# Kernel tuning notes

Hardware: AMD Instinct MI355X
Metric: run time of the kernel (lower is better)

The kernel has to match this reference:

```python
import jax, jax.numpy as jnp
import numpy as np

NUM_HEADS = 16
KEY_SIZE = 64
D_MODEL = 1024


def setup_inputs() -> dict:
    key = jax.random.key(0)
    ks = jax.random.split(key, 9)
    B, S = 2, 2048
    HK = NUM_HEADS * KEY_SIZE
    s = 1.0 / np.sqrt(D_MODEL)
    return {
        "x": jax.random.normal(ks[0], (B, S, D_MODEL), dtype=jnp.float32),
        "Wq": jax.random.normal(ks[1], (D_MODEL, HK), dtype=jnp.float32) * s,
        "bq": jax.random.normal(ks[2], (HK,), dtype=jnp.float32) * 0.02,
        "Wk": jax.random.normal(ks[3], (D_MODEL, HK), dtype=jnp.float32) * s,
        "bk": jax.random.normal(ks[4], (HK,), dtype=jnp.float32) * 0.02,
        "Wv": jax.random.normal(ks[5], (D_MODEL, HK), dtype=jnp.float32) * s,
        "bv": jax.random.normal(ks[6], (HK,), dtype=jnp.float32) * 0.02,
        "Wo": jax.random.normal(ks[7], (HK, D_MODEL), dtype=jnp.float32) * s,
        "bo": jax.random.normal(ks[8], (D_MODEL,), dtype=jnp.float32) * 0.02,
    }


def reference(x, Wq, bq, Wk, bk, Wv, bv, Wo, bo):
    B, S, _ = x.shape
    H, K = NUM_HEADS, KEY_SIZE
    # QKV projections -> (B, H, S, K)
    def proj(W, b):
        return (x @ W + b).reshape(B, S, H, K).transpose(0, 2, 1, 3)
    q = proj(Wq, bq)
    k = proj(Wk, bk)
    v = proj(Wv, bv)
    scale = jnp.sqrt(jnp.float32(K))
    scores = jnp.einsum('bhsk,bhtk->bhst', q, k) / scale  # (B,H,S,S)
    attn = jax.nn.softmax(scores, axis=-1)
    out = jnp.einsum('bhst,bhtk->bhsk', attn, v)  # (B,H,S,K)
    out = out.transpose(0, 2, 1, 3).reshape(B, S, H * K)
    return out @ Wo + bo
```

## Files before the change

### kernel.cpp

```cpp
#include <hip/hip_runtime.h>


#define NH 16
#define KS 64
#define DM 1024
#define BB 2
#define SS 2048
#define NT (BB*SS)
#define HKD 1024
#define L2E 1.44269504088896340736f

typedef __attribute__((ext_vector_type(4))) float floatx4;
typedef __attribute__((ext_vector_type(8))) short short8;

#define BAR() asm volatile("s_barrier" ::: "memory")

__device__ __forceinline__ unsigned short f2b(float f) {
  unsigned u = __builtin_bit_cast(unsigned, f);
  u = (u + 0x7fffu + ((u >> 16) & 1u)) >> 16;
  return (unsigned short)u;
}

__device__ __forceinline__ floatx4 mfma16(short8 a, short8 b, floatx4 c) {
  return __builtin_amdgcn_mfma_f32_16x16x32_bf16(a, b, c, 0, 0, 0);
}

__device__ __forceinline__ void async16(const void* g, void* l) {
  __builtin_amdgcn_global_load_lds(
      (const __attribute__((address_space(1))) unsigned int*)g,
      (__attribute__((address_space(3))) unsigned int*)l, 16, 0, 0);
}

__global__ __launch_bounds__(256) void prep_kernel(
    const float* __restrict__ x,
    const float* __restrict__ Wq, const float* __restrict__ Wk,
    const float* __restrict__ Wv, const float* __restrict__ Wo,
    unsigned short* __restrict__ xb,
    unsigned short* __restrict__ wqt, unsigned short* __restrict__ wkt,
    unsigned short* __restrict__ wvt, unsigned short* __restrict__ wot) {
  int bid = blockIdx.x;
  if (bid < NT * DM / 1024) {
    int i = (bid * 256 + threadIdx.x) * 4;
    float4 v = *(const float4*)(x + i);
    ushort4 o;
    o.x = f2b(v.x); o.y = f2b(v.y); o.z = f2b(v.z); o.w = f2b(v.w);
    *(ushort4*)(xb + i) = o;
    return;
  }
  int b2 = bid - NT * DM / 1024;
  int z = b2 >> 8;
  const float* W; unsigned short* Wt;
  if (z == 0)      { W = Wq; Wt = wqt; }
  else if (z == 1) { W = Wk; Wt = wkt; }
  else if (z == 2) { W = Wv; Wt = wvt; }
  else             { W = Wo; Wt = wot; }
  __shared__ __align__(16) unsigned short tile[64][80];
  int k0 = (b2 & 15) * 64, n0 = ((b2 >> 4) & 15) * 64;
  int t = threadIdx.x;
  int c0 = (t & 15) * 4, r = t >> 4;
  #pragma unroll
  for (int p = 0; p < 4; ++p) {
    int rr = r + p * 16;
    float4 v = *(const float4*)(W + (k0 + rr) * DM + n0 + c0);
    tile[c0 + 0][rr] = f2b(v.x);
    tile[c0 + 1][rr] = f2b(v.y);
    tile[c0 + 2][rr] = f2b(v.z);
    tile[c0 + 3][rr] = f2b(v.w);
  }
  __syncthreads();
  int cc0 = (t & 7) * 8, rn = t >> 3;
  #pragma unroll
  for (int p = 0; p < 2; ++p) {
    int nn = rn + p * 32;
    *(short8*)(Wt + (n0 + nn) * DM + k0 + cc0) = *(const short8*)(&tile[nn][cc0]);
  }
}

__global__ __launch_bounds__(256) void gemm_qkv_kernel(
    const unsigned short* __restrict__ xb,
    const unsigned short* __restrict__ wqt, const unsigned short* __restrict__ wkt,
    const unsigned short* __restrict__ wvt,
    const float* __restrict__ bq, const float* __restrict__ bk, const float* __restrict__ bv,
    unsigned short* __restrict__ qb, unsigned short* __restrict__ kbuf,
    unsigned short* __restrict__ vt) {
  __shared__ __align__(16) unsigned short smem[18432];
  const unsigned short* Bt; const float* bias; float scale; int zid = blockIdx.z;
  if (zid == 0)      { Bt = wqt; bias = bq; scale = 0.125f * L2E; }
  else if (zid == 1) { Bt = wkt; bias = bk; scale = 1.0f; }
  else               { Bt = wvt; bias = bv; scale = 1.0f; }
  int m0 = blockIdx.x * 128, n0 = blockIdx.y * 128;
  int t = threadIdx.x, w = t >> 6, lane = t & 63, cl = lane & 15, quad = lane >> 4;
  int wr = (w >> 1) * 64, wc = (w & 1) * 64;
  floatx4 acc[4][4];
  #pragma unroll
  for (int i = 0; i < 4; ++i)
    #pragma unroll
    for (int j = 0; j < 4; ++j)
      acc[i][j] = floatx4{0.f, 0.f, 0.f, 0.f};

  auto stage = [&](int kc, int buf) {
    #pragma unroll
    for (int i = 0; i < 2; ++i) {
      int c = i * 256 + t;
      int row = c >> 2, col = (c & 3) ^ (row & 3);
      async16(xb + (m0 + row) * DM + kc * 32 + col * 8, &smem[buf * 4096 + c * 8]);
      async16(Bt + (n0 + row) * DM + kc * 32 + col * 8, &smem[8192 + buf * 4096 + c * 8]);
    }
  };
  stage(0, 0);
  stage(1, 1);

  for (int kc = 0; kc < DM / 32; ++kc) {
    int cur = kc & 1;
    if (kc < DM / 32 - 1) asm volatile("s_waitcnt vmcnt(4)" ::: "memory");
    else                  asm volatile("s_waitcnt vmcnt(0)" ::: "memory");
    BAR();
    const unsigned short* Ac = &smem[cur * 4096];
    const unsigned short* Bc = &smem[8192 + cur * 4096];
    short8 a[4], b[4];
    #pragma unroll
    for (int i = 0; i < 4; ++i)
      a[i] = *(const short8*)&Ac[(wr + i * 16 + cl) * 32 + ((quad ^ (cl & 3)) * 8)];
    #pragma unroll
    for (int j = 0; j < 4; ++j)
      b[j] = *(const short8*)&Bc[(wc + j * 16 + cl) * 32 + ((quad ^ (cl & 3)) * 8)];
    #pragma unroll
    for (int i = 0; i < 4; ++i)
      #pragma unroll
      for (int j = 0; j < 4; ++j)
        acc[i][j] = mfma16(a[i], b[j], acc[i][j]);
    BAR();
    if (kc + 2 < DM / 32) stage(kc + 2, cur);
  }
  __syncthreads();

  int h = (n0 + wc) >> 6;
  if (zid < 2) {
    unsigned short* dst = (zid == 0) ? qb : kbuf;
    #pragma unroll
    for (int j = 0; j < 4; ++j) {
      float bj = bias[n0 + wc + j * 16 + cl];
      int kd = j * 16 + cl;
      #pragma unroll
      for (int i = 0; i < 4; ++i)
        #pragma unroll
        for (int r = 0; r < 4; ++r) {
          int token = m0 + wr + i * 16 + quad * 4 + r;
          int bz = token >> 11, s = token & (SS - 1);
          float val = (acc[i][j][r] + bj) * scale;
          dst[(((bz * NH + h) * SS + s) << 6) + kd] = f2b(val);
        }
    }
  } else {
    unsigned short* tr = &smem[w * 4608];
    #pragma unroll
    for (int j = 0; j < 4; ++j) {
      float bj = bias[n0 + wc + j * 16 + cl];
      #pragma unroll
      for (int i = 0; i < 4; ++i) {
        unsigned short b0 = f2b(acc[i][j][0] + bj), b1 = f2b(acc[i][j][1] + bj);
        unsigned short b2 = f2b(acc[i][j][2] + bj), b3 = f2b(acc[i][j][3] + bj);
        uint2 pk;
        pk.x = (unsigned)b0 | ((unsigned)b1 << 16);
        pk.y = (unsigned)b2 | ((unsigned)b3 << 16);
        *(uint2*)&tr[(j * 16 + cl) * 72 + i * 16 + quad * 4] = pk;
      }
    }
    asm volatile("s_waitcnt lgkmcnt(0)" ::: "memory");
    int tokbase = m0 + wr;
    int bz = tokbase >> 11, s0 = tokbase & (SS - 1);
    unsigned short* vdst = vt + (((bz * NH + h) * KS) * SS) + s0;
    #pragma unroll
    for (int p = 0; p < 8; ++p) {
      int row = p * 8 + (lane >> 3);
      int tk = (lane & 7) * 8;
      short8 vv = *(const short8*)&tr[row * 72 + tk];
      *(short8*)(vdst + row * SS + tk) = vv;
    }
  }
}

__global__ __launch_bounds__(256) void attn_kernel(
    const unsigned short* __restrict__ Q, const unsigned short* __restrict__ Kb,
    const unsigned short* __restrict__ Vt, unsigned short* __restrict__ AO) {
  __shared__ __align__(16) unsigned short Ks[2][4096], Vs[2][4096];
  __shared__ __align__(16) unsigned short Ps[4][2048];
  int t = threadIdx.x, w = t >> 6, lane = t & 63, cl = lane & 15, quad = lane >> 4;
  int clm = cl & 7;
  int h = blockIdx.y, bz = blockIdx.z, bh = bz * NH + h;
  int q0 = blockIdx.x * 128 + w * 32;
  const unsigned short* Qp = Q + (bh * SS + q0) * KS;
  const unsigned short* Kp = Kb + bh * SS * KS;
  const unsigned short* Vp = Vt + bh * KS * SS;
  unsigned short* p_w = Ps[w];

  short8 qa[2][2];
  #pragma unroll
  for (int qt = 0; qt < 2; ++qt)
    #pragma unroll
    for (int c = 0; c < 2; ++c)
      qa[qt][c] = *(const short8*)(Qp + (qt * 16 + cl) * KS + c * 32 + quad * 8);

  short8 ones;
  #pragma unroll
  for (int j = 0; j < 8; ++j) ones[j] = (short)0x3f80;

  floatx4 lacc[2];
  floatx4 oa[2][4];
  #pragma unroll
  for (int qt = 0; qt < 2; ++qt) {
    lacc[qt] = floatx4{0.f, 0.f, 0.f, 0.f};
    #pragma unroll
    for (int j = 0; j < 4; ++j) oa[qt][j] = floatx4{0.f, 0.f, 0.f, 0.f};
  }

  auto stage = [&](int tile, int buf) {
    #pragma unroll
    for (int i = 0; i < 2; ++i) {
      int c = i * 256 + t;
      int row = c >> 3, col8 = (c & 7) ^ (row & 7);
      async16(Kp + (tile * 64 + row) * KS + col8 * 8, &Ks[buf][c * 8]);
    }
    #pragma unroll
    for (int i = 0; i < 2; ++i) {
      int c = i * 256 + t;
      int d = c >> 3, col8 = (c & 7) ^ (d & 7);
      async16(Vp + d * SS + tile * 64 + col8 * 8, &Vs[buf][c * 8]);
    }
  };
  stage(0, 0);
  stage(1, 1);

  const int NTILES = SS / 64;
  for (int it = 0; it < NTILES; ++it) {
    int cur = it & 1;
    if (it < NTILES - 1) asm volatile("s_waitcnt vmcnt(4)" ::: "memory");
    else                 asm volatile("s_waitcnt vmcnt(0)" ::: "memory");
    BAR();

    floatx4 s[2][4];
    #pragma unroll
    for (int kt = 0; kt < 4; ++kt) {
      short8 kb0 = *(const short8*)&Ks[cur][(kt * 16 + cl) * 64 + ((quad ^ clm) * 8)];
      short8 kb1 = *(const short8*)&Ks[cur][(kt * 16 + cl) * 64 + (((4 + quad) ^ clm) * 8)];
      #pragma unroll
      for (int qt = 0; qt < 2; ++qt) {
        floatx4 z = {0.f, 0.f, 0.f, 0.f};
        s[qt][kt] = mfma16(kb1, qa[qt][1], mfma16(kb0, qa[qt][0], z));
      }
    }
    #pragma unroll
    for (int qt = 0; qt < 2; ++qt)
      #pragma unroll
      for (int kt = 0; kt < 4; ++kt) {
        unsigned u[4];
        #pragma unroll
        for (int r = 0; r < 4; ++r)
          u[r] = __builtin_bit_cast(unsigned, __builtin_amdgcn_exp2f(s[qt][kt][r]));
        uint2 pk;
        pk.x = __builtin_amdgcn_perm(u[1], u[0], 0x07060302);
        pk.y = __builtin_amdgcn_perm(u[3], u[2], 0x07060302);
        int off = qt * 1024 + cl * 64 + (((kt * 2 + (quad >> 1)) ^ clm) * 8) + (quad & 1) * 4;
        *(uint2*)(p_w + off) = pk;
      }
    asm volatile("s_waitcnt lgkmcnt(0)" ::: "memory");
    short8 pa[2][2];
    #pragma unroll
    for (int qt = 0; qt < 2; ++qt) {
      #pragma unroll
      for (int c = 0; c < 2; ++c)
        pa[qt][c] = *(const short8*)(p_w + qt * 1024 + cl * 64 + (((c * 4 + quad) ^ clm) * 8));
      lacc[qt] = mfma16(ones, pa[qt][1], mfma16(ones, pa[qt][0], lacc[qt]));
    }
    #pragma unroll
    for (int j = 0; j < 4; ++j) {
      short8 vb0 = *(const short8*)&Vs[cur][(j * 16 + cl) * 64 + ((quad ^ clm) * 8)];
      short8 vb1 = *(const short8*)&Vs[cur][(j * 16 + cl) * 64 + (((4 + quad) ^ clm) * 8)];
      #pragma unroll
      for (int qt = 0; qt < 2; ++qt)
        oa[qt][j] = mfma16(vb1, pa[qt][1], mfma16(vb0, pa[qt][0], oa[qt][j]));
    }
    BAR();
    if (it + 2 < NTILES) stage(it + 2, cur);
  }

  #pragma unroll
  for (int qt = 0; qt < 2; ++qt) {
    float inv = 1.0f / lacc[qt][0];
    unsigned short* aop = AO + (bz * SS + q0 + qt * 16 + cl) * DM + h * KS + quad * 4;
    #pragma unroll
    for (int j = 0; j < 4; ++j) {
      unsigned short b0 = f2b(oa[qt][j][0] * inv), b1 = f2b(oa[qt][j][1] * inv);
      unsigned short b2 = f2b(oa[qt][j][2] * inv), b3 = f2b(oa[qt][j][3] * inv);
      uint2 pk;
      pk.x = (unsigned)b0 | ((unsigned)b1 << 16);
      pk.y = (unsigned)b2 | ((unsigned)b3 << 16);
      *(uint2*)(aop + j * 16) = pk;
    }
  }
}

__global__ __launch_bounds__(256) void gemm_out_kernel(
    const unsigned short* __restrict__ ao, const unsigned short* __restrict__ wot,
    const float* __restrict__ bo, float* __restrict__ out) {
  __shared__ __align__(16) unsigned short As[2][8192], Bs[2][2048];
  int m0 = blockIdx.x * 256, n0 = blockIdx.y * 64;
  int t = threadIdx.x, w = t >> 6, lane = t & 63, cl = lane & 15, quad = lane >> 4;
  int wr = w * 64;
  floatx4 acc[4][4];
  #pragma unroll
  for (int i = 0; i < 4; ++i)
    #pragma unroll
    for (int j = 0; j < 4; ++j)
      acc[i][j] = floatx4{0.f, 0.f, 0.f, 0.f};

  auto stage = [&](int kc, int buf) {
    #pragma unroll
    for (int i = 0; i < 4; ++i) {
      int c = i * 256 + t;
      int row = c >> 2, col = (c & 3) ^ (row & 3);
      async16(ao + (m0 + row) * HKD + kc * 32 + col * 8, &As[buf][c * 8]);
    }
    {
      int c = t;
      int row = c >> 2, col = (c & 3) ^ (row & 3);
      async16(wot + (n0 + row) * HKD + kc * 32 + col * 8, &Bs[buf][c * 8]);
    }
  };
  stage(0, 0);
  stage(1, 1);

  for (int kc = 0; kc < HKD / 32; ++kc) {
    int cur = kc & 1;
    if (kc < HKD / 32 - 1) asm volatile("s_waitcnt vmcnt(5)" ::: "memory");
    else                   asm volatile("s_waitcnt vmcnt(0)" ::: "memory");
    BAR();
    short8 a[4], b[4];
    #pragma unroll
    for (int i = 0; i < 4; ++i)
      a[i] = *(const short8*)&As[cur][(wr + i * 16 + cl) * 32 + ((quad ^ (cl & 3)) * 8)];
    #pragma unroll
    for (int j = 0; j < 4; ++j)
      b[j] = *(const short8*)&Bs[cur][(j * 16 + cl) * 32 + ((quad ^ (cl & 3)) * 8)];
    #pragma unroll
    for (int i = 0; i < 4; ++i)
      #pragma unroll
      for (int j = 0; j < 4; ++j)
        acc[i][j] = mfma16(a[i], b[j], acc[i][j]);
    BAR();
    if (kc + 2 < HKD / 32) stage(kc + 2, cur);
  }
  #pragma unroll
  for (int j = 0; j < 4; ++j) {
    float bj = bo[n0 + j * 16 + cl];
    #pragma unroll
    for (int i = 0; i < 4; ++i)
      #pragma unroll
      for (int r = 0; r < 4; ++r) {
        int token = m0 + wr + i * 16 + quad * 4 + r;
        out[token * DM + n0 + j * 16 + cl] = acc[i][j][r] + bj;
      }
  }
}

extern "C" void kernel_launch(void* const* d_in, const int* in_sizes, int n_in,
                              void* d_out, int out_size, void* d_ws, size_t ws_size,
                              hipStream_t stream) {
  const float* x  = (const float*)d_in[0];
  const float* Wq = (const float*)d_in[1];
  const float* bq = (const float*)d_in[2];
  const float* Wk = (const float*)d_in[3];
  const float* bk = (const float*)d_in[4];
  const float* Wv = (const float*)d_in[5];
  const float* bv = (const float*)d_in[6];
  const float* Wo = (const float*)d_in[7];
  const float* bo = (const float*)d_in[8];
  float* out = (float*)d_out;
  char* ws = (char*)d_ws;
  unsigned short* xb  = (unsigned short*)(ws);
  unsigned short* wqt = (unsigned short*)(ws + (8ull  << 20));
  unsigned short* wkt = (unsigned short*)(ws + (10ull << 20));
  unsigned short* wvt = (unsigned short*)(ws + (12ull << 20));
  unsigned short* wot = (unsigned short*)(ws + (14ull << 20));
  unsigned short* qb  = (unsigned short*)(ws + (16ull << 20));
  unsigned short* kbf = (unsigned short*)(ws + (24ull << 20));
  unsigned short* vt  = (unsigned short*)(ws + (40ull << 20));
  unsigned short* ao  = (unsigned short*)(ws + (48ull << 20));

  hipLaunchKernelGGL(prep_kernel, dim3(NT * DM / 1024 + 1024), dim3(256), 0, stream,
                     x, Wq, Wk, Wv, Wo, xb, wqt, wkt, wvt, wot);
  hipLaunchKernelGGL(gemm_qkv_kernel, dim3(NT / 128, HKD / 128, 3), dim3(256), 0, stream,
                     xb, wqt, wkt, wvt, bq, bk, bv, qb, kbf, vt);
  hipLaunchKernelGGL(attn_kernel, dim3(SS / 128, NH, BB), dim3(256), 0, stream, qb, kbf, vt, ao);
  hipLaunchKernelGGL(gemm_out_kernel, dim3(NT / 256, DM / 64), dim3(256), 0, stream, ao, wot, bo, out);
}
```

Measured before the change: 202.2 us.

## Split attention key range across two wave groups with LDS reduction

The attention kernel now runs 512 threads per block. Two groups of four waves each process half of the key sequence for the same 128 queries, using 32-key tiles. At the end the partial outputs and row sums are combined through shared memory before normalization. The aim is more waves in flight to hide latency, since the grid of 512 blocks is small relative to the CU count. The cost is an extra LDS reduction and barrier, smaller tiles per iteration, and possibly lower occupancy per CU.

Measured after the change: 197.7 us. 2.2% less time.

```diff
diff --git a/kernel.cpp b/kernel.cpp
--- a/kernel.cpp
+++ b/kernel.cpp
@@ -180,19 +180,19 @@
   }
 }
 
-__global__ __launch_bounds__(256) void attn_kernel(
+__global__ __launch_bounds__(512) void attn_kernel(
     const unsigned short* __restrict__ Q, const unsigned short* __restrict__ Kb,
     const unsigned short* __restrict__ Vt, unsigned short* __restrict__ AO) {
-  __shared__ __align__(16) unsigned short Ks[2][4096], Vs[2][4096];
-  __shared__ __align__(16) unsigned short Ps[4][2048];
+  __shared__ __align__(16) unsigned short smem[24576];
   int t = threadIdx.x, w = t >> 6, lane = t & 63, cl = lane & 15, quad = lane >> 4;
-  int clm = cl & 7;
+  int clm = cl & 7, cl3 = cl & 3, cl2 = cl >> 2;
   int h = blockIdx.y, bz = blockIdx.z, bh = bz * NH + h;
-  int q0 = blockIdx.x * 128 + w * 32;
+  int slice = w & 3, part = w >> 2;
+  int q0 = blockIdx.x * 128 + slice * 32;
   const unsigned short* Qp = Q + (bh * SS + q0) * KS;
   const unsigned short* Kp = Kb + bh * SS * KS;
   const unsigned short* Vp = Vt + bh * KS * SS;
-  unsigned short* p_w = Ps[w];
+  unsigned short* p_w = smem + 16384 + w * 1024;
 
   short8 qa[2][2];
   #pragma unroll
@@ -214,35 +214,32 @@
     for (int j = 0; j < 4; ++j) oa[qt][j] = floatx4{0.f, 0.f, 0.f, 0.f};
   }
 
-  auto stage = [&](int tile, int buf) {
-    #pragma unroll
-    for (int i = 0; i < 2; ++i) {
-      int c = i * 256 + t;
-      int row = c >> 3, col8 = (c & 7) ^ (row & 7);
-      async16(Kp + (tile * 64 + row) * KS + col8 * 8, &Ks[buf][c * 8]);
-    }
-    #pragma unroll
-    for (int i = 0; i < 2; ++i) {
-      int c = i * 256 + t;
-      int d = c >> 3, col8 = (c & 7) ^ (d & 7);
-      async16(Vp + d * SS + tile * 64 + col8 * 8, &Vs[buf][c * 8]);
-    }
+  int st = t >> 8, lt = t & 255;
+  int krow = lt >> 3, kcol = (lt & 7) ^ (krow & 7);
+  int vd = lt >> 2, vcol = ((lt & 3) ^ (vd & 3) ^ ((vd >> 2) & 3)) & 3;
+  auto stage = [&](int it, int buf) {
+    async16(Kp + (st * 1024 + it * 32 + krow) * KS + kcol * 8,
+            &smem[(st * 2 + buf) * 2048 + lt * 8]);
+    async16(Vp + vd * SS + st * 1024 + it * 32 + vcol * 8,
+            &smem[8192 + (st * 2 + buf) * 2048 + lt * 8]);
   };
   stage(0, 0);
   stage(1, 1);
 
-  const int NTILES = SS / 64;
-  for (int it = 0; it < NTILES; ++it) {
+  const int NIT = 1024 / 32;
+  for (int it = 0; it < NIT; ++it) {
     int cur = it & 1;
-    if (it < NTILES - 1) asm volatile("s_waitcnt vmcnt(4)" ::: "memory");
-    else                 asm volatile("s_waitcnt vmcnt(0)" ::: "memory");
-    BAR();
-
-    floatx4 s[2][4];
-    #pragma unroll
-    for (int kt = 0; kt < 4; ++kt) {
-      short8 kb0 = *(const short8*)&Ks[cur][(kt * 16 + cl) * 64 + ((quad ^ clm) * 8)];
-      short8 kb1 = *(const short8*)&Ks[cur][(kt * 16 + cl) * 64 + (((4 + quad) ^ clm) * 8)];
+    if (it < NIT - 1) asm volatile("s_waitcnt vmcnt(2)" ::: "memory");
+    else              asm volatile("s_waitcnt vmcnt(0)" ::: "memory");
+    BAR();
+    const unsigned short* Kc = &smem[(part * 2 + cur) * 2048];
+    const unsigned short* Vc = &smem[8192 + (part * 2 + cur) * 2048];
+
+    floatx4 s[2][2];
+    #pragma unroll
+    for (int kt = 0; kt < 2; ++kt) {
+      short8 kb0 = *(const short8*)&Kc[(kt * 16 + cl) * 64 + ((quad ^ clm) * 8)];
+      short8 kb1 = *(const short8*)&Kc[(kt * 16 + cl) * 64 + (((4 + quad) ^ clm) * 8)];
       #pragma unroll
       for (int qt = 0; qt < 2; ++qt) {
         floatx4 z = {0.f, 0.f, 0.f, 0.f};
@@ -252,7 +249,7 @@
     #pragma unroll
     for (int qt = 0; qt < 2; ++qt)
       #pragma unroll
-      for (int kt = 0; kt < 4; ++kt) {
+      for (int kt = 0; kt < 2; ++kt) {
         unsigned u[4];
         #pragma unroll
         for (int r = 0; r < 4; ++r)
@@ -260,42 +257,63 @@
         uint2 pk;
         pk.x = __builtin_amdgcn_perm(u[1], u[0], 0x07060302);
         pk.y = __builtin_amdgcn_perm(u[3], u[2], 0x07060302);
-        int off = qt * 1024 + cl * 64 + (((kt * 2 + (quad >> 1)) ^ clm) * 8) + (quad & 1) * 4;
+        int blk = ((kt * 2 + (quad >> 1)) ^ cl3 ^ cl2) & 3;
+        int off = qt * 512 + cl * 32 + blk * 8 + (quad & 1) * 4;
         *(uint2*)(p_w + off) = pk;
       }
     asm volatile("s_waitcnt lgkmcnt(0)" ::: "memory");
-    short8 pa[2][2];
+    short8 pa[2];
     #pragma unroll
     for (int qt = 0; qt < 2; ++qt) {
-      #pragma unroll
-      for (int c = 0; c < 2; ++c)
-        pa[qt][c] = *(const short8*)(p_w + qt * 1024 + cl * 64 + (((c * 4 + quad) ^ clm) * 8));
-      lacc[qt] = mfma16(ones, pa[qt][1], mfma16(ones, pa[qt][0], lacc[qt]));
+      pa[qt] = *(const short8*)(p_w + qt * 512 + cl * 32 + (((quad ^ cl3 ^ cl2) & 3) * 8));
+      lacc[qt] = mfma16(ones, pa[qt], lacc[qt]);
     }
     #pragma unroll
     for (int j = 0; j < 4; ++j) {
-      short8 vb0 = *(const short8*)&Vs[cur][(j * 16 + cl) * 64 + ((quad ^ clm) * 8)];
-      short8 vb1 = *(const short8*)&Vs[cur][(j * 16 + cl) * 64 + (((4 + quad) ^ clm) * 8)];
+      short8 vb = *(const short8*)&Vc[(j * 16 + cl) * 32 + (((quad ^ cl3 ^ cl2) & 3) * 8)];
       #pragma unroll
       for (int qt = 0; qt < 2; ++qt)
-        oa[qt][j] = mfma16(vb1, pa[qt][1], mfma16(vb0, pa[qt][0], oa[qt][j]));
-    }
-    BAR();
-    if (it + 2 < NTILES) stage(it + 2, cur);
-  }
-
-  #pragma unroll
-  for (int qt = 0; qt < 2; ++qt) {
-    float inv = 1.0f / lacc[qt][0];
-    unsigned short* aop = AO + (bz * SS + q0 + qt * 16 + cl) * DM + h * KS + quad * 4;
-    #pragma unroll
-    for (int j = 0; j < 4; ++j) {
-      unsigned short b0 = f2b(oa[qt][j][0] * inv), b1 = f2b(oa[qt][j][1] * inv);
-      unsigned short b2 = f2b(oa[qt][j][2] * inv), b3 = f2b(oa[qt][j][3] * inv);
-      uint2 pk;
-      pk.x = (unsigned)b0 | ((unsigned)b1 << 16);
-      pk.y = (unsigned)b2 | ((unsigned)b3 << 16);
-      *(uint2*)(aop + j * 16) = pk;
+        oa[qt][j] = mfma16(vb, pa[qt], oa[qt][j]);
+    }
+    BAR();
+    if (it + 2 < NIT) stage(it + 2, cur);
+  }
+
+  __syncthreads();
+  float* red = (float*)smem;
+  float* base = red + slice * 2304;
+  if (part == 1) {
+    #pragma unroll
+    for (int qt = 0; qt < 2; ++qt)
+      #pragma unroll
+      for (int j = 0; j < 4; ++j)
+        *(floatx4*)(base + (((qt * 4 + j) * 64 + lane) << 2)) = oa[qt][j];
+    base[2048 + lane * 2 + 0] = lacc[0][0];
+    base[2048 + lane * 2 + 1] = lacc[1][0];
+  }
+  __syncthreads();
+  if (part == 0) {
+    #pragma unroll
+    for (int qt = 0; qt < 2; ++qt)
+      #pragma unroll
+      for (int j = 0; j < 4; ++j)
+        oa[qt][j] += *(const floatx4*)(base + (((qt * 4 + j) * 64 + lane) << 2));
+    float lsum[2];
+    lsum[0] = lacc[0][0] + base[2048 + lane * 2 + 0];
+    lsum[1] = lacc[1][0] + base[2048 + lane * 2 + 1];
+    #pragma unroll
+    for (int qt = 0; qt < 2; ++qt) {
+      float inv = 1.0f / lsum[qt];
+      unsigned short* aop = AO + (bz * SS + q0 + qt * 16 + cl) * DM + h * KS + quad * 4;
+      #pragma unroll
+      for (int j = 0; j < 4; ++j) {
+        unsigned short b0 = f2b(oa[qt][j][0] * inv), b1 = f2b(oa[qt][j][1] * inv);
+        unsigned short b2 = f2b(oa[qt][j][2] * inv), b3 = f2b(oa[qt][j][3] * inv);
+        uint2 pk;
+        pk.x = (unsigned)b0 | ((unsigned)b1 << 16);
+        pk.y = (unsigned)b2 | ((unsigned)b3 << 16);
+        *(uint2*)(aop + j * 16) = pk;
+      }
     }
   }
 }
@@ -391,6 +409,6 @@
                      x, Wq, Wk, Wv, Wo, xb, wqt, wkt, wvt, wot);
   hipLaunchKernelGGL(gemm_qkv_kernel, dim3(NT / 128, HKD / 128, 3), dim3(256), 0, stream,
                      xb, wqt, wkt, wvt, bq, bk, bv, qb, kbf, vt);
-  hipLaunchKernelGGL(attn_kernel, dim3(SS / 128, NH, BB), dim3(256), 0, stream, qb, kbf, vt, ao);
+  hipLaunchKernelGGL(attn_kernel, dim3(SS / 128, NH, BB), dim3(512), 0, stream, qb, kbf, vt, ao);
   hipLaunchKernelGGL(gemm_out_kernel, dim3(NT / 256, DM / 64), dim3(256), 0, stream, ao, wot, bo, out);
 }
```
